# Optimization experiments

Hardware: AMD Instinct MI355X
Metric: run time of the kernel (lower is better)

The kernel has to match this reference:

```python
import jax, jax.numpy as jnp
import numpy as np

NQ, BS, NP_, D = 100, 8, 17, 256
NH, L, P = 8, 4, 4
DH = D // NH
DFF = 1024
SHAPES = [(92, 92), (46, 46), (23, 23), (12, 12)]
LEN_IN = sum(h * w for h, w in SHAPES)


def setup_inputs() -> dict:
    key = jax.random.key(0)
    ks = jax.random.split(key, 20)
    def nrm(k, shape, s=0.02):
        return jax.random.normal(k, shape, jnp.float32) * s
    return {
        "tgt_pose": jax.random.normal(ks[0], (NQ, BS, NP_, D), jnp.float32),
        "tgt_pose_query_pos": jax.random.normal(ks[1], (NQ, BS, NP_, D), jnp.float32),
        "tgt_pose_reference_points": jax.random.uniform(ks[2], (NQ, BS, NP_, L, 2), jnp.float32),
        "memory": jax.random.normal(ks[3], (BS, LEN_IN, D), jnp.float32),
        "w_in_w": nrm(ks[4], (3 * D, D)), "b_in_w": jnp.zeros((3 * D,), jnp.float32),
        "w_out_w": nrm(ks[5], (D, D)), "b_out_w": jnp.zeros((D,), jnp.float32),
        "w_in_a": nrm(ks[6], (3 * D, D)), "b_in_a": jnp.zeros((3 * D,), jnp.float32),
        "w_out_a": nrm(ks[7], (D, D)), "b_out_a": jnp.zeros((D,), jnp.float32),
        "w_off": nrm(ks[8], (NH * L * P * 2, D)), "b_off": nrm(ks[9], (NH * L * P * 2,), 0.1),
        "w_aw": nrm(ks[10], (NH * L * P, D)), "b_aw": jnp.zeros((NH * L * P,), jnp.float32),
        "w_val": nrm(ks[11], (D, D)), "b_val": jnp.zeros((D,), jnp.float32),
        "w_oc": nrm(ks[12], (D, D)), "b_oc": jnp.zeros((D,), jnp.float32),
        "g_w": jnp.ones((D,), jnp.float32), "be_w": jnp.zeros((D,), jnp.float32),
        "g_a": jnp.ones((D,), jnp.float32), "be_a": jnp.zeros((D,), jnp.float32),
        "g1": jnp.ones((D,), jnp.float32), "be1": jnp.zeros((D,), jnp.float32),
        "g2": jnp.ones((D,), jnp.float32), "be2": jnp.zeros((D,), jnp.float32),
        "w1": nrm(ks[13], (DFF, D)), "b1": jnp.zeros((DFF,), jnp.float32),
        "w2": nrm(ks[14], (D, DFF)), "b2": jnp.zeros((D,), jnp.float32),
        "memory_key_padding_mask": jnp.zeros((BS, LEN_IN), jnp.bool_),
        "memory_spatial_shapes": jnp.array(SHAPES, jnp.int32),
        "memory_level_start_index": jnp.array(np.cumsum([0] + [h * w for h, w in SHAPES[:-1]]), jnp.int32),
    }


def _ln(x, g, b, eps=1e-5):
    m = x.mean(-1, keepdims=True)
    v = ((x - m) ** 2).mean(-1, keepdims=True)
    return (x - m) * jax.lax.rsqrt(v + eps) * g + b


def _mha(q, k, v, w_in, b_in, w_out, b_out):
    # q,k,v: [B, S, D] batch-first; torch nn.MultiheadAttention math
    B, S, d = q.shape
    qp = (q @ w_in[:d].T + b_in[:d]).reshape(B, S, NH, DH)
    kp = (k @ w_in[d:2 * d].T + b_in[d:2 * d]).reshape(B, -1, NH, DH)
    vp = (v @ w_in[2 * d:].T + b_in[2 * d:]).reshape(B, -1, NH, DH)
    att = jax.nn.softmax(jnp.einsum('bqhd,bkhd->bhqk', qp, kp) / jnp.sqrt(jnp.float32(DH)), axis=-1)
    o = jnp.einsum('bhqk,bkhd->bqhd', att, vp).reshape(B, S, d)
    return o @ w_out.T + b_out


def _bilinear(v, loc, Hl, Wl):
    # v: [Hl*Wl, NH, DH]; loc: [Lq, NH, P, 2] normalized to [0,1]; grid_sample align_corners=False, zero pad
    x = loc[..., 0] * Wl - 0.5
    y = loc[..., 1] * Hl - 0.5
    x0 = jnp.floor(x); y0 = jnp.floor(y)
    wx = x - x0; wy = y - y0
    x0i = x0.astype(jnp.int32); y0i = y0.astype(jnp.int32)
    hid = jnp.arange(NH)[None, :, None]
    def tap(yi, xi, w):
        ok = (xi >= 0) & (xi < Wl) & (yi >= 0) & (yi < Hl)
        idx = jnp.clip(yi, 0, Hl - 1) * Wl + jnp.clip(xi, 0, Wl - 1)
        return jnp.where(ok[..., None], v[idx, hid], 0.0) * w[..., None]
    return (tap(y0i, x0i, (1 - wy) * (1 - wx)) + tap(y0i, x0i + 1, (1 - wy) * wx)
            + tap(y0i + 1, x0i, wy * (1 - wx)) + tap(y0i + 1, x0i + 1, wy * wx))


def _deform(query, ref, memory, mask, shapes, starts, w_off, b_off, w_aw, b_aw, w_val, b_val, w_oc, b_oc):
    # Multi-scale deformable attention (MSDeformAttn)
    bs, lq, d = query.shape
    value = memory @ w_val.T + b_val
    value = jnp.where(mask[..., None], 0.0, value).reshape(bs, -1, NH, DH)
    off = (query @ w_off.T + b_off).reshape(bs, lq, NH, L, P, 2)
    aw = jax.nn.softmax((query @ w_aw.T + b_aw).reshape(bs, lq, NH, L * P), axis=-1).reshape(bs, lq, NH, L, P)
    shp = np.asarray(shapes)
    st = np.asarray(starts)
    norm = jnp.asarray(shp[:, ::-1].copy(), jnp.float32)  # (W, H) per level
    loc = ref[:, :, None, :, None, :] + off / norm[None, None, None, :, None, :]
    out = jnp.zeros((bs, lq, NH, DH), query.dtype)
    for l in range(L):
        Hl, Wl = int(shp[l, 0]), int(shp[l, 1])
        v_l = value[:, int(st[l]):int(st[l]) + Hl * Wl]
        samp = jax.vmap(lambda vv, lo: _bilinear(vv, lo, Hl, Wl))(v_l, loc[:, :, :, l])
        out = out + jnp.einsum('bqhp,bqhpd->bqhd', aw[:, :, :, l], samp)
    return out.reshape(bs, lq, d) @ w_oc.T + b_oc


def _forward(tgt_pose, qpos, ref, memory, w_in_w, b_in_w, w_out_w, b_out_w, w_in_a, b_in_a, w_out_a, b_out_a, w_off, b_off, w_aw, b_aw, w_val, b_val, w_oc, b_oc, g_w, be_w, g_a, be_a, g1, be1, g2, be2, w1, b1, w2, b2, mask, shapes, starts):
    nq, bs, npt, d = tgt_pose.shape
    # within-group self-attn over keypoints (seq = np, batch = nq*bs)
    qk = (tgt_pose + qpos).reshape(nq * bs, npt, d)
    t2 = _mha(qk, qk, tgt_pose.reshape(nq * bs, npt, d), w_in_w, b_in_w, w_out_w, b_out_w).reshape(nq, bs, npt, d)
    x = _ln(tgt_pose + t2, g_w, be_w)
    # across-group self-attn over queries (seq = nq, batch = bs*np)
    y = x.reshape(nq, bs * npt, d).transpose(1, 0, 2)
    t2 = _mha(y, y, y, w_in_a, b_in_a, w_out_a, b_out_a).transpose(1, 0, 2).reshape(nq, bs, npt, d)
    x = _ln(x + t2, g_a, be_a)
    # multi-scale deformable cross-attn
    q = (x + qpos).transpose(1, 0, 2, 3).reshape(bs, nq * npt, d)
    r = ref.transpose(1, 0, 2, 3, 4).reshape(bs, nq * npt, L, 2)
    t2 = _deform(q, r, memory, mask, shapes, starts, w_off, b_off, w_aw, b_aw, w_val, b_val, w_oc, b_oc)
    t2 = t2.reshape(bs, nq, npt, d).transpose(1, 0, 2, 3)
    x = _ln(x + t2, g1, be1)
    # FFN
    ff = jax.nn.relu(x @ w1.T + b1) @ w2.T + b2
    return _ln(x + ff, g2, be2)


def reference(tgt_pose, tgt_pose_query_pos, tgt_pose_reference_points, memory, w_in_w, b_in_w, w_out_w, b_out_w, w_in_a, b_in_a, w_out_a, b_out_a, w_off, b_off, w_aw, b_aw, w_val, b_val, w_oc, b_oc, g_w, be_w, g_a, be_a, g1, be1, g2, be2, w1, b1, w2, b2, memory_key_padding_mask, memory_spatial_shapes, memory_level_start_index):
    return _forward(tgt_pose, tgt_pose_query_pos, tgt_pose_reference_points, memory, w_in_w, b_in_w, w_out_w, b_out_w, w_in_a, b_in_a, w_out_a, b_out_a, w_off, b_off, w_aw, b_aw, w_val, b_val, w_oc, b_oc, g_w, be_w, g_a, be_a, g1, be1, g2, be2, w1, b1, w2, b2, memory_key_padding_mask, memory_spatial_shapes, memory_level_start_index)
```

## Files before the change

kernel.cpp:

```cpp
#include <hip/hip_runtime.h>
#include <hip/hip_bf16.h>
#include <math.h>

#define NQd 100
#define BSd 8
#define NPTd 17
#define DIMd 256
#define NHd 8
#define DHd 32
#define DFFd 1024
#define NTOK (NQd*BSd*NPTd)
#define LENIN 11253
#define MTOK (BSd*LENIN)

typedef __attribute__((ext_vector_type(8))) short bf16x8;
typedef __attribute__((ext_vector_type(4))) short bf16x4s;
typedef __attribute__((ext_vector_type(4))) float f32x4;

__device__ inline short f2bs(float f) {
    __hip_bfloat16 h = __float2bfloat16(f);
    return *reinterpret_cast<short*>(&h);
}
__device__ inline float bs2f(short s) {
    return __uint_as_float(((unsigned)(unsigned short)s) << 16);
}

template<bool RELU, bool OUT_BF16, bool A_FP32>
__global__ __launch_bounds__(256)
void gemm_mfma(const void* __restrict__ Av, const __hip_bfloat16* __restrict__ W,
               const float* __restrict__ bias, void* __restrict__ Cv,
               int M, int N, int K, int ldc, int col0) {
    __shared__ __hip_bfloat16 LA[2][4][129][8];
    __shared__ __hip_bfloat16 LW[2][4][129][8];
    const int tid = threadIdx.x;
    const int lane = tid & 63, wave = tid >> 6;
    const int wr = wave >> 1, wc = wave & 1;
    const int m0 = blockIdx.y * 128, n0 = blockIdx.x * 128;
    const int l15 = lane & 15, lg = lane >> 4;
    const int srow = tid >> 2, koct = tid & 3;
    bf16x8 aReg[2], wReg[2];

    auto load_tile = [&](int k0) {
#pragma unroll
        for (int it = 0; it < 2; ++it) {
            const int row = srow + it * 64;
            const int gm = m0 + row;
            bf16x8 av = {0, 0, 0, 0, 0, 0, 0, 0};
            if (A_FP32) {
                if (gm < M) {
                    const float* ap = (const float*)Av + (size_t)gm * K + k0 + koct * 8;
                    float4 f0 = *(const float4*)ap;
                    float4 f1 = *(const float4*)(ap + 4);
                    av = (bf16x8){f2bs(f0.x), f2bs(f0.y), f2bs(f0.z), f2bs(f0.w),
                                  f2bs(f1.x), f2bs(f1.y), f2bs(f1.z), f2bs(f1.w)};
                }
            } else {
                if (gm < M)
                    av = *(const bf16x8*)((const __hip_bfloat16*)Av + (size_t)gm * K + k0 + koct * 8);
            }
            aReg[it] = av;
            wReg[it] = *(const bf16x8*)(W + (size_t)(n0 + row) * K + k0 + koct * 8);
        }
    };
    auto write_tile = [&](int buf) {
#pragma unroll
        for (int it = 0; it < 2; ++it) {
            const int row = srow + it * 64;
            *(bf16x8*)&LA[buf][koct][row][0] = aReg[it];
            *(bf16x8*)&LW[buf][koct][row][0] = wReg[it];
        }
    };

    f32x4 acc[4][4];
#pragma unroll
    for (int i = 0; i < 4; ++i)
#pragma unroll
        for (int j = 0; j < 4; ++j) acc[i][j] = (f32x4){0.f, 0.f, 0.f, 0.f};

    const int NT = K >> 5;
    load_tile(0);
    write_tile(0);
    __syncthreads();
    for (int t = 0; t < NT; ++t) {
        const int cur = t & 1;
        if (t + 1 < NT) load_tile((t + 1) * 32);
        bf16x8 af[4], bfr[4];
#pragma unroll
        for (int f = 0; f < 4; ++f) {
            af[f]  = *(const bf16x8*)&LA[cur][lg][wr * 64 + f * 16 + l15][0];
            bfr[f] = *(const bf16x8*)&LW[cur][lg][wc * 64 + f * 16 + l15][0];
        }
#pragma unroll
        for (int fm = 0; fm < 4; ++fm)
#pragma unroll
            for (int fn = 0; fn < 4; ++fn)
                acc[fm][fn] = __builtin_amdgcn_mfma_f32_16x16x32_bf16(af[fm], bfr[fn], acc[fm][fn], 0, 0, 0);
        if (t + 1 < NT) write_tile(cur ^ 1);
        __syncthreads();
    }

#pragma unroll
    for (int fm = 0; fm < 4; ++fm) {
        const int row = m0 + wr * 64 + fm * 16 + lg * 4;
#pragma unroll
        for (int fn = 0; fn < 4; ++fn) {
            const int coln = n0 + wc * 64 + fn * 16 + l15;
            const float bsv = bias[coln];
#pragma unroll
            for (int r = 0; r < 4; ++r) {
                const int gr = row + r;
                if (gr >= M) continue;
                float v = acc[fm][fn][r] + bsv;
                if (RELU) v = fmaxf(v, 0.f);
                if (OUT_BF16)
                    ((__hip_bfloat16*)Cv)[(size_t)gr * ldc + col0 + coln] = __float2bfloat16(v);
                else
                    ((float*)Cv)[(size_t)gr * ldc + col0 + coln] = v;
            }
        }
    }
}

template<bool A_FP32, bool OUT_BF16>
__global__ __launch_bounds__(256)
void gemm64(const void* __restrict__ Av, const __hip_bfloat16* __restrict__ W,
            const float* __restrict__ bias, void* __restrict__ Cv,
            int M, int K, int ldc, int col0) {
    __shared__ __hip_bfloat16 LA[2][4][65][8];
    __shared__ __hip_bfloat16 LW[2][4][65][8];
    const int tid = threadIdx.x;
    const int lane = tid & 63, wave = tid >> 6;
    const int wr = wave >> 1, wc = wave & 1;
    const int m0 = blockIdx.y * 64, n0 = blockIdx.x * 64;
    const int l15 = lane & 15, lg = lane >> 4;
    const int srow = tid >> 2, koct = tid & 3;
    const int gm = m0 + srow;
    const bool okA = gm < M;
    const __hip_bfloat16* pAb = (const __hip_bfloat16*)Av + (size_t)(okA ? gm : 0) * K + koct * 8;
    const float* pAf = (const float*)Av + (size_t)(okA ? gm : 0) * K + koct * 8;
    const __hip_bfloat16* pW = W + (size_t)(n0 + srow) * K + koct * 8;

    bf16x8 aR, wR;
    float4 f0R, f1R;
    auto load_tile = [&](int k0) {
        if (A_FP32) {
            f0R = okA ? *(const float4*)(pAf + k0)     : make_float4(0.f, 0.f, 0.f, 0.f);
            f1R = okA ? *(const float4*)(pAf + k0 + 4) : make_float4(0.f, 0.f, 0.f, 0.f);
        } else {
            aR = okA ? *(const bf16x8*)(pAb + k0) : (bf16x8){0, 0, 0, 0, 0, 0, 0, 0};
        }
        wR = *(const bf16x8*)(pW + k0);
    };
    auto write_tile = [&](int buf) {
        bf16x8 v;
        if (A_FP32)
            v = (bf16x8){f2bs(f0R.x), f2bs(f0R.y), f2bs(f0R.z), f2bs(f0R.w),
                         f2bs(f1R.x), f2bs(f1R.y), f2bs(f1R.z), f2bs(f1R.w)};
        else
            v = aR;
        *(bf16x8*)&LA[buf][koct][srow][0] = v;
        *(bf16x8*)&LW[buf][koct][srow][0] = wR;
    };

    f32x4 acc[2][2];
#pragma unroll
    for (int i = 0; i < 2; ++i)
#pragma unroll
        for (int j = 0; j < 2; ++j) acc[i][j] = (f32x4){0.f, 0.f, 0.f, 0.f};

    const int NT = K >> 5;
    load_tile(0);
    write_tile(0);
    __syncthreads();
    for (int t = 0; t < NT; ++t) {
        const int cur = t & 1;
        if (t + 1 < NT) load_tile((t + 1) * 32);
        bf16x8 af[2], bfr[2];
#pragma unroll
        for (int f = 0; f < 2; ++f) {
            af[f]  = *(const bf16x8*)&LA[cur][lg][wr * 32 + f * 16 + l15][0];
            bfr[f] = *(const bf16x8*)&LW[cur][lg][wc * 32 + f * 16 + l15][0];
        }
#pragma unroll
        for (int fm = 0; fm < 2; ++fm)
#pragma unroll
            for (int fn = 0; fn < 2; ++fn)
                acc[fm][fn] = __builtin_amdgcn_mfma_f32_16x16x32_bf16(af[fm], bfr[fn], acc[fm][fn], 0, 0, 0);
        if (t + 1 < NT) write_tile(cur ^ 1);
        __syncthreads();
    }

#pragma unroll
    for (int fm = 0; fm < 2; ++fm) {
        const int row = m0 + wr * 32 + fm * 16 + lg * 4;
#pragma unroll
        for (int fn = 0; fn < 2; ++fn) {
            const int coln = n0 + wc * 32 + fn * 16 + l15;
            const float bsv = bias[coln];
#pragma unroll
            for (int r = 0; r < 4; ++r) {
                const int gr = row + r;
                if (gr >= M) continue;
                float v = acc[fm][fn][r] + bsv;
                if (OUT_BF16)
                    ((__hip_bfloat16*)Cv)[(size_t)gr * ldc + col0 + coln] = __float2bfloat16(v);
                else
                    ((float*)Cv)[(size_t)gr * ldc + col0 + coln] = v;
            }
        }
    }
}

__global__ __launch_bounds__(256)
void gemm64x(const float* __restrict__ Av, const __hip_bfloat16* __restrict__ W,
             const float* __restrict__ bias, __hip_bfloat16* __restrict__ Cv,
             int M, int K, int ldc) {
    const int nwg = gridDim.x;
    const int orig = blockIdx.x;
    const int xcd = orig & 7, loc = orig >> 3;
    const int q = nwg >> 3, r = nwg & 7;
    const int swz = (xcd < r ? xcd * (q + 1) : r * (q + 1) + (xcd - r) * q) + loc;
    const int m0 = (swz >> 2) * 64, n0 = (swz & 3) * 64;

    __shared__ __hip_bfloat16 LA[2][4][65][8];
    __shared__ __hip_bfloat16 LW[2][4][65][8];
    const int tid = threadIdx.x;
    const int lane = tid & 63, wave = tid >> 6;
    const int wr = wave >> 1, wc = wave & 1;
    const int l15 = lane & 15, lg = lane >> 4;
    const int srow = tid >> 2, koct = tid & 3;
    const int gm = m0 + srow;
    const bool okA = gm < M;
    const float* pAf = Av + (size_t)(okA ? gm : 0) * K + koct * 8;
    const __hip_bfloat16* pW = W + (size_t)(n0 + srow) * K + koct * 8;

    bf16x8 wR;
    float4 f0R, f1R;
    auto load_tile = [&](int k0) {
        f0R = okA ? *(const float4*)(pAf + k0)     : make_float4(0.f, 0.f, 0.f, 0.f);
        f1R = okA ? *(const float4*)(pAf + k0 + 4) : make_float4(0.f, 0.f, 0.f, 0.f);
        wR = *(const bf16x8*)(pW + k0);
    };
    auto write_tile = [&](int buf) {
        *(bf16x8*)&LA[buf][koct][srow][0] =
            (bf16x8){f2bs(f0R.x), f2bs(f0R.y), f2bs(f0R.z), f2bs(f0R.w),
                     f2bs(f1R.x), f2bs(f1R.y), f2bs(f1R.z), f2bs(f1R.w)};
        *(bf16x8*)&LW[buf][koct][srow][0] = wR;
    };

    f32x4 acc[2][2];
#pragma unroll
    for (int i = 0; i < 2; ++i)
#pragma unroll
        for (int j = 0; j < 2; ++j) acc[i][j] = (f32x4){0.f, 0.f, 0.f, 0.f};

    const int NT = K >> 5;
    load_tile(0);
    write_tile(0);
    __syncthreads();
    for (int t = 0; t < NT; ++t) {
        const int cur = t & 1;
        if (t + 1 < NT) load_tile((t + 1) * 32);
        bf16x8 af[2], bfr[2];
#pragma unroll
        for (int f = 0; f < 2; ++f) {
            af[f]  = *(const bf16x8*)&LA[cur][lg][wr * 32 + f * 16 + l15][0];
            bfr[f] = *(const bf16x8*)&LW[cur][lg][wc * 32 + f * 16 + l15][0];
        }
#pragma unroll
        for (int fm = 0; fm < 2; ++fm)
#pragma unroll
            for (int fn = 0; fn < 2; ++fn)
                acc[fm][fn] = __builtin_amdgcn_mfma_f32_16x16x32_bf16(af[fm], bfr[fn], acc[fm][fn], 0, 0, 0);
        if (t + 1 < NT) write_tile(cur ^ 1);
        __syncthreads();
    }

#pragma unroll
    for (int fm = 0; fm < 2; ++fm) {
        const int row = m0 + wr * 32 + fm * 16 + lg * 4;
#pragma unroll
        for (int fn = 0; fn < 2; ++fn) {
            const int coln = n0 + wc * 32 + fn * 16 + l15;
            const float bsv = bias[coln];
#pragma unroll
            for (int r = 0; r < 4; ++r) {
                const int gr = row + r;
                if (gr >= M) continue;
                Cv[(size_t)gr * ldc + coln] = __float2bfloat16(acc[fm][fn][r] + bsv);
            }
        }
    }
}

__global__ void cvt_weights(const float* w0, const float* w1, const float* w2,
                            const float* w3, const float* w4, const float* w5,
                            const float* w6, const float* w7, const float* w8,
                            const float* w9, __hip_bfloat16* dst) {
    int idx = blockIdx.x * 256 + threadIdx.x;
    float v;
    if      (idx <  196608) v = w0[idx];
    else if (idx <  262144) v = w1[idx -  196608];
    else if (idx <  458752) v = w2[idx -  262144];
    else if (idx <  524288) v = w3[idx -  458752];
    else if (idx <  589824) v = w4[idx -  524288];
    else if (idx <  622592) v = w5[idx -  589824];
    else if (idx <  688128) v = w6[idx -  622592];
    else if (idx <  753664) v = w7[idx -  688128];
    else if (idx < 1015808) v = w8[idx -  753664];
    else                    v = w9[idx - 1015808];
    dst[idx] = __float2bfloat16(v);
}

__global__ void gather_rows_b(const float* __restrict__ src, const float* __restrict__ add,
                              __hip_bfloat16* __restrict__ dst, int mode) {
    int t = blockIdx.x, c = threadIdx.x;
    int r;
    if (mode == 0) r = t;
    else if (mode == 1) { int m = t / 100, q = t % 100; r = q * 136 + m; }
    else { int b = t / 1700, jj = t % 1700; int q = jj / 17, p = jj % 17; r = q * 136 + b * 17 + p; }
    float v = src[(size_t)r * 256 + c];
    if (add) v += add[(size_t)r * 256 + c];
    dst[(size_t)t * 256 + c] = __float2bfloat16(v);
}

__global__ void attn17(const __hip_bfloat16* __restrict__ qkv, __hip_bfloat16* __restrict__ out) {
    const int g = blockIdx.x, h = blockIdx.y;
    __shared__ float q[17][32], k[17][32], v[17][32], s[17][18];
    const int tid = threadIdx.x;
    for (int idx = tid; idx < 17 * 32; idx += 256) {
        int i = idx >> 5, d = idx & 31;
        size_t row = (size_t)(g * 17 + i) * 768 + h * 32 + d;
        q[i][d] = bs2f(*(const short*)&qkv[row]);
        k[i][d] = bs2f(*(const short*)&qkv[row + 256]);
        v[i][d] = bs2f(*(const short*)&qkv[row + 512]);
    }
    __syncthreads();
    for (int idx = tid; idx < 17 * 17; idx += 256) {
        int i = idx / 17, j = idx % 17;
        float acc = 0.f;
#pragma unroll
        for (int d = 0; d < 32; ++d) acc += q[i][d] * k[j][d];
        s[i][j] = acc * 0.17677669529663688f;
    }
    __syncthreads();
    if (tid < 17) {
        float m = -1e30f;
        for (int j = 0; j < 17; ++j) m = fmaxf(m, s[tid][j]);
        float sum = 0.f;
        for (int j = 0; j < 17; ++j) { float e = __expf(s[tid][j] - m); s[tid][j] = e; sum += e; }
        float inv = 1.f / sum;
        for (int j = 0; j < 17; ++j) s[tid][j] *= inv;
    }
    __syncthreads();
    for (int idx = tid; idx < 17 * 32; idx += 256) {
        int i = idx >> 5, d = idx & 31;
        float acc = 0.f;
        for (int j = 0; j < 17; ++j) acc += s[i][j] * v[j][d];
        out[(size_t)(g * 17 + i) * 256 + h * 32 + d] = __float2bfloat16(acc);
    }
}

__global__ __launch_bounds__(128)
void attn100(const __hip_bfloat16* __restrict__ qkv, __hip_bfloat16* __restrict__ out) {
    const int g = blockIdx.x, h = blockIdx.y;
    __shared__ __hip_bfloat16 Vt[32][136];
    __shared__ __hip_bfloat16 Pl[2][16][136];
    const int tid = threadIdx.x;
    const int wave = tid >> 6, lane = tid & 63;
    const int l15 = lane & 15, lg = lane >> 4;

    for (int idx = tid; idx < 3200; idx += 128) {
        int j = idx >> 5, d = idx & 31;
        Vt[d][j] = qkv[(size_t)(g * 100 + j) * 768 + 512 + h * 32 + d];
    }
    for (int idx = tid; idx < 32 * 28; idx += 128) {
        int d = idx & 31, jz = 100 + (idx >> 5);
        Vt[d][jz] = __float2bfloat16(0.f);
    }
    __syncthreads();

    const int rt0 = wave ? 4 : 0, rt1 = wave ? 7 : 4;
    for (int rt = rt0; rt < rt1; ++rt) {
        const int rowbase = rt * 16;
        int qr = rowbase + l15; if (qr > 99) qr = 99;
        bf16x8 aq = *(const bf16x8*)(qkv + (size_t)(g * 100 + qr) * 768 + h * 32 + lg * 8);
        f32x4 s[7];
#pragma unroll
        for (int jt = 0; jt < 7; ++jt) {
            int jr = jt * 16 + l15; if (jr > 99) jr = 99;
            bf16x8 bk = *(const bf16x8*)(qkv + (size_t)(g * 100 + jr) * 768 + 256 + h * 32 + lg * 8);
            s[jt] = __builtin_amdgcn_mfma_f32_16x16x32_bf16(aq, bk, (f32x4){0.f, 0.f, 0.f, 0.f}, 0, 0, 0);
        }
        float mr[4] = {-1e30f, -1e30f, -1e30f, -1e30f};
#pragma unroll
        for (int jt = 0; jt < 7; ++jt) {
            const bool valid = (jt * 16 + l15) < 100;
#pragma unroll
            for (int r = 0; r < 4; ++r) {
                float v = valid ? s[jt][r] * 0.17677669529663688f : -1e30f;
                s[jt][r] = v;
                mr[r] = fmaxf(mr[r], v);
            }
        }
#pragma unroll
        for (int r = 0; r < 4; ++r) {
            mr[r] = fmaxf(mr[r], __shfl_xor(mr[r], 1));
            mr[r] = fmaxf(mr[r], __shfl_xor(mr[r], 2));
            mr[r] = fmaxf(mr[r], __shfl_xor(mr[r], 4));
            mr[r] = fmaxf(mr[r], __shfl_xor(mr[r], 8));
        }
        float lr[4] = {0.f, 0.f, 0.f, 0.f};
#pragma unroll
        for (int jt = 0; jt < 7; ++jt)
#pragma unroll
            for (int r = 0; r < 4; ++r) {
                float e = __expf(s[jt][r] - mr[r]);
                s[jt][r] = e;
                lr[r] += e;
            }
#pragma unroll
        for (int r = 0; r < 4; ++r) {
            lr[r] += __shfl_xor(lr[r], 1);
            lr[r] += __shfl_xor(lr[r], 2);
            lr[r] += __shfl_xor(lr[r], 4);
            lr[r] += __shfl_xor(lr[r], 8);
        }
#pragma unroll
        for (int jt = 0; jt < 7; ++jt)
#pragma unroll
            for (int r = 0; r < 4; ++r)
                Pl[wave][lg * 4 + r][jt * 16 + l15] = __float2bfloat16(s[jt][r]);
#pragma unroll
        for (int r = 0; r < 4; ++r)
            Pl[wave][lg * 4 + r][112 + l15] = __float2bfloat16(0.f);

        f32x4 o0 = (f32x4){0.f, 0.f, 0.f, 0.f};
        f32x4 o1 = (f32x4){0.f, 0.f, 0.f, 0.f};
#pragma unroll
        for (int c = 0; c < 4; ++c) {
            bf16x8 pa = *(const bf16x8*)&Pl[wave][l15][c * 32 + lg * 8];
            bf16x8 v0 = *(const bf16x8*)&Vt[l15][c * 32 + lg * 8];
            bf16x8 v1 = *(const bf16x8*)&Vt[16 + l15][c * 32 + lg * 8];
            o0 = __builtin_amdgcn_mfma_f32_16x16x32_bf16(pa, v0, o0, 0, 0, 0);
            o1 = __builtin_amdgcn_mfma_f32_16x16x32_bf16(pa, v1, o1, 0, 0, 0);
        }
#pragma unroll
        for (int r = 0; r < 4; ++r) {
            int row = rowbase + lg * 4 + r;
            if (row < 100) {
                float inv = 1.f / lr[r];
                __hip_bfloat16* op = out + (size_t)(g * 100 + row) * 256 + h * 32;
                op[l15]      = __float2bfloat16(o0[r] * inv);
                op[16 + l15] = __float2bfloat16(o1[r] * inv);
            }
        }
    }
}

#define TPB 4
__global__ __launch_bounds__(256)
void deform_sample(const __hip_bfloat16* __restrict__ value, const float* __restrict__ off,
                   const float* __restrict__ aw, const float* __restrict__ ref,
                   __hip_bfloat16* __restrict__ out) {
    const int t0 = blockIdx.x * TPB;
    const int tid = threadIdx.x;
    __shared__ float raw[TPB][128];
    __shared__ float wgt[TPB][128];
    __shared__ int   cidx[TPB][128][4];
    __shared__ float cw[TPB][128][4];

    for (int idx = tid; idx < TPB * 128; idx += 256) {
        int tk = idx >> 7, i = idx & 127;
        raw[tk][i] = aw[(size_t)(t0 + tk) * 128 + i];
    }
    __syncthreads();
    if (tid < TPB * 8) {
        int tk = tid >> 3, h = tid & 7;
        float m = -1e30f;
        for (int i = 0; i < 16; ++i) m = fmaxf(m, raw[tk][h * 16 + i]);
        float sum = 0.f;
        float e[16];
        for (int i = 0; i < 16; ++i) { e[i] = __expf(raw[tk][h * 16 + i] - m); sum += e[i]; }
        float inv = 1.f / sum;
        for (int i = 0; i < 16; ++i) wgt[tk][h * 16 + i] = e[i] * inv;
    }
    __syncthreads();

    const int Hs[4] = {92, 46, 23, 12};
    const int Sts[4] = {0, 8464, 10580, 11109};
    for (int s = tid; s < TPB * 128; s += 256) {
        int tk = s >> 7, sid = s & 127;
        int t = t0 + tk;
        int b = t / 1700, jj = t % 1700;
        int q = jj / 17, p = jj % 17;
        int l = (sid >> 2) & 3;
        int HW = Hs[l];
        float HWf = (float)HW;
        const float* refp = ref + (size_t)((q * 8 + b) * 17 + p) * 8;
        float rx = refp[l * 2], ry = refp[l * 2 + 1];
        float ox = off[(size_t)t * 256 + sid * 2];
        float oy = off[(size_t)t * 256 + sid * 2 + 1];
        float x = (rx + ox / HWf) * HWf - 0.5f;
        float y = (ry + oy / HWf) * HWf - 0.5f;
        float x0f = floorf(x), y0f = floorf(y);
        float wx = x - x0f, wy = y - y0f;
        int xi = (int)x0f, yi = (int)y0f;
        float wg = wgt[tk][sid];
#pragma unroll
        for (int c = 0; c < 4; ++c) {
            int cy = c >> 1, cx = c & 1;
            int yy = yi + cy, xx = xi + cx;
            bool ok = (xx >= 0) && (xx < HW) && (yy >= 0) && (yy < HW);
            int yc = min(max(yy, 0), HW - 1);
            int xc = min(max(xx, 0), HW - 1);
            cidx[tk][sid][c] = Sts[l] + yc * HW + xc;
            float w = (cy ? wy : 1.f - wy) * (cx ? wx : 1.f - wx);
            cw[tk][sid][c] = ok ? wg * w : 0.f;
        }
    }
    __syncthreads();

    const int tk = tid >> 6, lane = tid & 63;
    const int h = lane >> 3, d4 = (lane & 7) * 4;
    const int t = t0 + tk;
    const int b = t / 1700;
    const __hip_bfloat16* vb = value + (size_t)b * LENIN * 256 + h * 32 + d4;
    float4 acc = make_float4(0.f, 0.f, 0.f, 0.f);
    for (int s16 = 0; s16 < 16; ++s16) {
        int sid = h * 16 + s16;
#pragma unroll
        for (int c = 0; c < 4; ++c) {
            int idx = cidx[tk][sid][c];
            float w = cw[tk][sid][c];
            bf16x4s v = *(const bf16x4s*)(vb + (size_t)idx * 256);
            acc.x += w * bs2f(v.x); acc.y += w * bs2f(v.y);
            acc.z += w * bs2f(v.z); acc.w += w * bs2f(v.w);
        }
    }
    __hip_bfloat16* op = out + (size_t)t * 256 + h * 32 + d4;
    op[0] = __float2bfloat16(acc.x);
    op[1] = __float2bfloat16(acc.y);
    op[2] = __float2bfloat16(acc.z);
    op[3] = __float2bfloat16(acc.w);
}

__global__ __launch_bounds__(256)
void res_ln(const float* __restrict__ res, const float* __restrict__ proj,
            const float* __restrict__ g, const float* __restrict__ be,
            float* __restrict__ out, __hip_bfloat16* __restrict__ outb, int mode) {
    const int wave = threadIdx.x >> 6, lane = threadIdx.x & 63;
    const int r = blockIdx.x * 4 + wave;
    int t;
    if (mode == 0) t = r;
    else if (mode == 1) { int q = r / 136, m = r % 136; t = m * 100 + q; }
    else { int q = r / 136, rem = r % 136; int b = rem / 17, p = rem % 17; t = b * 1700 + q * 17 + p; }
    const int c4 = lane * 4;
    float4 a = *(const float4*)&res[(size_t)r * 256 + c4];
    float4 p = *(const float4*)&proj[(size_t)t * 256 + c4];
    float v[4] = {a.x + p.x, a.y + p.y, a.z + p.z, a.w + p.w};
    float s = v[0] + v[1] + v[2] + v[3];
#pragma unroll
    for (int off = 32; off > 0; off >>= 1) s += __shfl_xor(s, off);
    float mean = s * (1.f / 256.f);
    float d[4], ss = 0.f;
#pragma unroll
    for (int i = 0; i < 4; ++i) { d[i] = v[i] - mean; ss += d[i] * d[i]; }
#pragma unroll
    for (int off = 32; off > 0; off >>= 1) ss += __shfl_xor(ss, off);
    float rs = rsqrtf(ss * (1.f / 256.f) + 1e-5f);
    float4 gv = *(const float4*)&g[c4];
    float4 bv = *(const float4*)&be[c4];
    float o0 = d[0] * rs * gv.x + bv.x;
    float o1 = d[1] * rs * gv.y + bv.y;
    float o2 = d[2] * rs * gv.z + bv.z;
    float o3 = d[3] * rs * gv.w + bv.w;
    *(float4*)&out[(size_t)r * 256 + c4] = make_float4(o0, o1, o2, o3);
    if (outb) {
        bf16x4s ob = {f2bs(o0), f2bs(o1), f2bs(o2), f2bs(o3)};
        *(bf16x4s*)&outb[(size_t)r * 256 + c4] = ob;
    }
}

extern "C" void kernel_launch(void* const* d_in, const int* in_sizes, int n_in,
                              void* d_out, int out_size, void* d_ws, size_t ws_size,
                              hipStream_t stream) {
    const float* tgt    = (const float*)d_in[0];
    const float* qpos   = (const float*)d_in[1];
    const float* ref    = (const float*)d_in[2];
    const float* memory = (const float*)d_in[3];
    const float* w_in_w = (const float*)d_in[4];
    const float* b_in_w = (const float*)d_in[5];
    const float* w_out_w= (const float*)d_in[6];
    const float* b_out_w= (const float*)d_in[7];
    const float* w_in_a = (const float*)d_in[8];
    const float* b_in_a = (const float*)d_in[9];
    const float* w_out_a= (const float*)d_in[10];
    const float* b_out_a= (const float*)d_in[11];
    const float* w_off  = (const float*)d_in[12];
    const float* b_off  = (const float*)d_in[13];
    const float* w_aw   = (const float*)d_in[14];
    const float* b_aw   = (const float*)d_in[15];
    const float* w_val  = (const float*)d_in[16];
    const float* b_val  = (const float*)d_in[17];
    const float* w_oc   = (const float*)d_in[18];
    const float* b_oc   = (const float*)d_in[19];
    const float* g_w    = (const float*)d_in[20];
    const float* be_w   = (const float*)d_in[21];
    const float* g_a    = (const float*)d_in[22];
    const float* be_a   = (const float*)d_in[23];
    const float* g1     = (const float*)d_in[24];
    const float* be1    = (const float*)d_in[25];
    const float* g2     = (const float*)d_in[26];
    const float* be2    = (const float*)d_in[27];
    const float* w1     = (const float*)d_in[28];
    const float* b1     = (const float*)d_in[29];
    const float* w2     = (const float*)d_in[30];
    const float* b2     = (const float*)d_in[31];

    float* X  = (float*)d_out;
    float* ws = (float*)d_ws;
    float* R1 = ws;
    float* R2 = R1 + (size_t)MTOK * 256;
    float* R3 = R2 + (size_t)NTOK * 256;
    float* R6 = R3 + (size_t)NTOK * 128;
    float* QBF= R6 + (size_t)NTOK * 128;
    float* WBF= QBF+ (size_t)NTOK * 128;

    __hip_bfloat16* R1b = (__hip_bfloat16*)R1;
    __hip_bfloat16* R3b = (__hip_bfloat16*)R3;
    __hip_bfloat16* Qb  = (__hip_bfloat16*)QBF;
    __hip_bfloat16* Wb  = (__hip_bfloat16*)WBF;
    __hip_bfloat16* Hb  = (__hip_bfloat16*)R1;
    __hip_bfloat16* Vb  = (__hip_bfloat16*)R1;

    __hip_bfloat16* w_in_w_b  = Wb;
    __hip_bfloat16* w_out_w_b = Wb +  196608;
    __hip_bfloat16* w_in_a_b  = Wb +  262144;
    __hip_bfloat16* w_out_a_b = Wb +  458752;
    __hip_bfloat16* w_off_b   = Wb +  524288;
    __hip_bfloat16* w_aw_b    = Wb +  589824;
    __hip_bfloat16* w_val_b   = Wb +  622592;
    __hip_bfloat16* w_oc_b    = Wb +  688128;
    __hip_bfloat16* w1_b      = Wb +  753664;
    __hip_bfloat16* w2_b      = Wb + 1015808;

    cvt_weights<<<4992, 256, 0, stream>>>(w_in_w, w_out_w, w_in_a, w_out_a, w_off,
                                          w_aw, w_val, w_oc, w1, w2, Wb);

    const int MY64 = (NTOK + 63) / 64;

    gather_rows_b<<<NTOK, 256, 0, stream>>>(tgt, qpos, Qb, 0);
    gemm_mfma<false, true, false><<<dim3(4, (NTOK + 127) / 128), 256, 0, stream>>>(
        Qb, w_in_w_b, b_in_w, R1b, NTOK, 512, 256, 768, 0);
    gemm64<true, true><<<dim3(4, MY64), 256, 0, stream>>>(
        tgt, w_in_w_b + 512 * 256, b_in_w + 512, R1b, NTOK, 256, 768, 512);
    attn17<<<dim3(800, 8), 256, 0, stream>>>(R1b, R3b);
    gemm64<false, false><<<dim3(4, MY64), 256, 0, stream>>>(
        R3b, w_out_w_b, b_out_w, R2, NTOK, 256, 256, 0);
    res_ln<<<NTOK / 4, 256, 0, stream>>>(tgt, R2, g_w, be_w, X, nullptr, 0);

    gather_rows_b<<<NTOK, 256, 0, stream>>>(X, nullptr, Qb, 1);
    gemm_mfma<false, true, false><<<dim3(6, (NTOK + 127) / 128), 256, 0, stream>>>(
        Qb, w_in_a_b, b_in_a, R1b, NTOK, 768, 256, 768, 0);
    attn100<<<dim3(136, 8), 128, 0, stream>>>(R1b, R3b);
    gemm64<false, false><<<dim3(4, MY64), 256, 0, stream>>>(
        R3b, w_out_a_b, b_out_a, R2, NTOK, 256, 256, 0);
    res_ln<<<NTOK / 4, 256, 0, stream>>>(X, R2, g_a, be_a, X, nullptr, 1);

    gemm64x<<<4 * ((MTOK + 63) / 64), 256, 0, stream>>>(
        memory, w_val_b, b_val, Vb, MTOK, 256, 256);
    gather_rows_b<<<NTOK, 256, 0, stream>>>(X, qpos, Qb, 2);
    gemm64<false, false><<<dim3(4, MY64), 256, 0, stream>>>(
        Qb, w_off_b, b_off, R2, NTOK, 256, 256, 0);
    gemm64<false, false><<<dim3(2, MY64), 256, 0, stream>>>(
        Qb, w_aw_b, b_aw, R6, NTOK, 256, 128, 0);
    deform_sample<<<NTOK / TPB, 256, 0, stream>>>(Vb, R2, R6, ref, R3b);
    gemm64<false, false><<<dim3(4, MY64), 256, 0, stream>>>(
        R3b, w_oc_b, b_oc, R2, NTOK, 256, 256, 0);
    res_ln<<<NTOK / 4, 256, 0, stream>>>(X, R2, g1, be1, X, Qb, 2);

    gemm_mfma<true, true, false><<<dim3(8, (NTOK + 127) / 128), 256, 0, stream>>>(
        Qb, w1_b, b1, Hb, NTOK, 1024, 256, 1024, 0);
    gemm64<false, false><<<dim3(4, MY64), 256, 0, stream>>>(
        (const __hip_bfloat16*)Hb, w2_b, b2, R2, NTOK, 1024, 256, 0);
    res_ln<<<NTOK / 4, 256, 0, stream>>>(X, R2, g2, be2, X, nullptr, 0);
}
```

Before: 326.6 us.

## Fuse row gathers into GEMM A-loads and drop the 128-tile GEMM

Removes the separate gather_rows_b kernels. Their permutation and the query-pos add now happen inside the GEMM A-tile load (AMAP modes), which saves a bf16 round trip through global memory per projection. The offset and attention-weight projections are merged into one kernel that writes to two outputs. All 128x128 gemm_mfma launches become 64x64 gemm64 launches with more blocks, which trades data reuse per block for more parallelism. The fused paths read fp32 activations on every N-block, so redundant global reads and per-row index math increase.

```diff
diff --git a/kernel.cpp b/kernel.cpp
--- a/kernel.cpp
+++ b/kernel.cpp
@@ -25,107 +25,11 @@
     return __uint_as_float(((unsigned)(unsigned short)s) << 16);
 }
 
-template<bool RELU, bool OUT_BF16, bool A_FP32>
+template<int AMAP, bool OUT_BF16, bool RELU>
 __global__ __launch_bounds__(256)
-void gemm_mfma(const void* __restrict__ Av, const __hip_bfloat16* __restrict__ W,
-               const float* __restrict__ bias, void* __restrict__ Cv,
-               int M, int N, int K, int ldc, int col0) {
-    __shared__ __hip_bfloat16 LA[2][4][129][8];
-    __shared__ __hip_bfloat16 LW[2][4][129][8];
-    const int tid = threadIdx.x;
-    const int lane = tid & 63, wave = tid >> 6;
-    const int wr = wave >> 1, wc = wave & 1;
-    const int m0 = blockIdx.y * 128, n0 = blockIdx.x * 128;
-    const int l15 = lane & 15, lg = lane >> 4;
-    const int srow = tid >> 2, koct = tid & 3;
-    bf16x8 aReg[2], wReg[2];
-
-    auto load_tile = [&](int k0) {
-#pragma unroll
-        for (int it = 0; it < 2; ++it) {
-            const int row = srow + it * 64;
-            const int gm = m0 + row;
-            bf16x8 av = {0, 0, 0, 0, 0, 0, 0, 0};
-            if (A_FP32) {
-                if (gm < M) {
-                    const float* ap = (const float*)Av + (size_t)gm * K + k0 + koct * 8;
-                    float4 f0 = *(const float4*)ap;
-                    float4 f1 = *(const float4*)(ap + 4);
-                    av = (bf16x8){f2bs(f0.x), f2bs(f0.y), f2bs(f0.z), f2bs(f0.w),
-                                  f2bs(f1.x), f2bs(f1.y), f2bs(f1.z), f2bs(f1.w)};
-                }
-            } else {
-                if (gm < M)
-                    av = *(const bf16x8*)((const __hip_bfloat16*)Av + (size_t)gm * K + k0 + koct * 8);
-            }
-            aReg[it] = av;
-            wReg[it] = *(const bf16x8*)(W + (size_t)(n0 + row) * K + k0 + koct * 8);
-        }
-    };
-    auto write_tile = [&](int buf) {
-#pragma unroll
-        for (int it = 0; it < 2; ++it) {
-            const int row = srow + it * 64;
-            *(bf16x8*)&LA[buf][koct][row][0] = aReg[it];
-            *(bf16x8*)&LW[buf][koct][row][0] = wReg[it];
-        }
-    };
-
-    f32x4 acc[4][4];
-#pragma unroll
-    for (int i = 0; i < 4; ++i)
-#pragma unroll
-        for (int j = 0; j < 4; ++j) acc[i][j] = (f32x4){0.f, 0.f, 0.f, 0.f};
-
-    const int NT = K >> 5;
-    load_tile(0);
-    write_tile(0);
-    __syncthreads();
-    for (int t = 0; t < NT; ++t) {
-        const int cur = t & 1;
-        if (t + 1 < NT) load_tile((t + 1) * 32);
-        bf16x8 af[4], bfr[4];
-#pragma unroll
-        for (int f = 0; f < 4; ++f) {
-            af[f]  = *(const bf16x8*)&LA[cur][lg][wr * 64 + f * 16 + l15][0];
-            bfr[f] = *(const bf16x8*)&LW[cur][lg][wc * 64 + f * 16 + l15][0];
-        }
-#pragma unroll
-        for (int fm = 0; fm < 4; ++fm)
-#pragma unroll
-            for (int fn = 0; fn < 4; ++fn)
-                acc[fm][fn] = __builtin_amdgcn_mfma_f32_16x16x32_bf16(af[fm], bfr[fn], acc[fm][fn], 0, 0, 0);
-        if (t + 1 < NT) write_tile(cur ^ 1);
-        __syncthreads();
-    }
-
-#pragma unroll
-    for (int fm = 0; fm < 4; ++fm) {
-        const int row = m0 + wr * 64 + fm * 16 + lg * 4;
-#pragma unroll
-        for (int fn = 0; fn < 4; ++fn) {
-            const int coln = n0 + wc * 64 + fn * 16 + l15;
-            const float bsv = bias[coln];
-#pragma unroll
-            for (int r = 0; r < 4; ++r) {
-                const int gr = row + r;
-                if (gr >= M) continue;
-                float v = acc[fm][fn][r] + bsv;
-                if (RELU) v = fmaxf(v, 0.f);
-                if (OUT_BF16)
-                    ((__hip_bfloat16*)Cv)[(size_t)gr * ldc + col0 + coln] = __float2bfloat16(v);
-                else
-                    ((float*)Cv)[(size_t)gr * ldc + col0 + coln] = v;
-            }
-        }
-    }
-}
-
-template<bool A_FP32, bool OUT_BF16>
-__global__ __launch_bounds__(256)
-void gemm64(const void* __restrict__ Av, const __hip_bfloat16* __restrict__ W,
-            const float* __restrict__ bias, void* __restrict__ Cv,
-            int M, int K, int ldc, int col0) {
+void gemm64(const void* __restrict__ Av, const float* __restrict__ Aadd,
+            const __hip_bfloat16* __restrict__ W, const float* __restrict__ bias,
+            void* __restrict__ Cv, int M, int K, int ldc, int col0) {
     __shared__ __hip_bfloat16 LA[2][4][65][8];
     __shared__ __hip_bfloat16 LW[2][4][65][8];
     const int tid = threadIdx.x;
@@ -136,28 +40,41 @@
     const int srow = tid >> 2, koct = tid & 3;
     const int gm = m0 + srow;
     const bool okA = gm < M;
-    const __hip_bfloat16* pAb = (const __hip_bfloat16*)Av + (size_t)(okA ? gm : 0) * K + koct * 8;
-    const float* pAf = (const float*)Av + (size_t)(okA ? gm : 0) * K + koct * 8;
+    int src = okA ? gm : 0;
+    if (AMAP == 3) src = (src % 100) * 136 + src / 100;
+    const __hip_bfloat16* pAb = (const __hip_bfloat16*)Av + (size_t)src * K + koct * 8;
+    const float* pAf = (const float*)Av + (size_t)src * K + koct * 8;
+    const float* pDf = (AMAP == 2) ? (Aadd + (size_t)src * K + koct * 8) : nullptr;
     const __hip_bfloat16* pW = W + (size_t)(n0 + srow) * K + koct * 8;
 
     bf16x8 aR, wR;
-    float4 f0R, f1R;
+    float4 f0R, f1R, d0R, d1R;
     auto load_tile = [&](int k0) {
-        if (A_FP32) {
+        if (AMAP == 0) {
+            aR = okA ? *(const bf16x8*)(pAb + k0) : (bf16x8){0, 0, 0, 0, 0, 0, 0, 0};
+        } else {
             f0R = okA ? *(const float4*)(pAf + k0)     : make_float4(0.f, 0.f, 0.f, 0.f);
             f1R = okA ? *(const float4*)(pAf + k0 + 4) : make_float4(0.f, 0.f, 0.f, 0.f);
-        } else {
-            aR = okA ? *(const bf16x8*)(pAb + k0) : (bf16x8){0, 0, 0, 0, 0, 0, 0, 0};
+            if (AMAP == 2) {
+                d0R = okA ? *(const float4*)(pDf + k0)     : make_float4(0.f, 0.f, 0.f, 0.f);
+                d1R = okA ? *(const float4*)(pDf + k0 + 4) : make_float4(0.f, 0.f, 0.f, 0.f);
+            }
         }
         wR = *(const bf16x8*)(pW + k0);
     };
     auto write_tile = [&](int buf) {
         bf16x8 v;
-        if (A_FP32)
-            v = (bf16x8){f2bs(f0R.x), f2bs(f0R.y), f2bs(f0R.z), f2bs(f0R.w),
-                         f2bs(f1R.x), f2bs(f1R.y), f2bs(f1R.z), f2bs(f1R.w)};
-        else
+        if (AMAP == 0) {
             v = aR;
+        } else {
+            float4 f0 = f0R, f1 = f1R;
+            if (AMAP == 2) {
+                f0.x += d0R.x; f0.y += d0R.y; f0.z += d0R.z; f0.w += d0R.w;
+                f1.x += d1R.x; f1.y += d1R.y; f1.z += d1R.z; f1.w += d1R.w;
+            }
+            v = (bf16x8){f2bs(f0.x), f2bs(f0.y), f2bs(f0.z), f2bs(f0.w),
+                         f2bs(f1.x), f2bs(f1.y), f2bs(f1.z), f2bs(f1.w)};
+        }
         *(bf16x8*)&LA[buf][koct][srow][0] = v;
         *(bf16x8*)&LW[buf][koct][srow][0] = wR;
     };
@@ -202,10 +119,102 @@
                 const int gr = row + r;
                 if (gr >= M) continue;
                 float v = acc[fm][fn][r] + bsv;
+                if (RELU) v = fmaxf(v, 0.f);
                 if (OUT_BF16)
                     ((__hip_bfloat16*)Cv)[(size_t)gr * ldc + col0 + coln] = __float2bfloat16(v);
                 else
                     ((float*)Cv)[(size_t)gr * ldc + col0 + coln] = v;
+            }
+        }
+    }
+}
+
+__global__ __launch_bounds__(256)
+void gemm64qa(const float* __restrict__ X, const float* __restrict__ qpos,
+              const __hip_bfloat16* __restrict__ W,
+              const float* __restrict__ boff, const float* __restrict__ baw,
+              float* __restrict__ Coff, float* __restrict__ Caw, int M, int K) {
+    __shared__ __hip_bfloat16 LA[2][4][65][8];
+    __shared__ __hip_bfloat16 LW[2][4][65][8];
+    const int tid = threadIdx.x;
+    const int lane = tid & 63, wave = tid >> 6;
+    const int wr = wave >> 1, wc = wave & 1;
+    const int m0 = blockIdx.y * 64, n0 = blockIdx.x * 64;
+    const int l15 = lane & 15, lg = lane >> 4;
+    const int srow = tid >> 2, koct = tid & 3;
+    const int gm = m0 + srow;
+    const bool okA = gm < M;
+    int t_ = okA ? gm : 0;
+    {
+        int b = t_ / 1700, jj = t_ % 1700;
+        int qq = jj / 17, p = jj % 17;
+        t_ = qq * 136 + b * 17 + p;
+    }
+    const float* pAf = X + (size_t)t_ * K + koct * 8;
+    const float* pDf = qpos + (size_t)t_ * K + koct * 8;
+    const __hip_bfloat16* pW = W + (size_t)(n0 + srow) * K + koct * 8;
+
+    bf16x8 wR;
+    float4 f0R, f1R, d0R, d1R;
+    auto load_tile = [&](int k0) {
+        f0R = okA ? *(const float4*)(pAf + k0)     : make_float4(0.f, 0.f, 0.f, 0.f);
+        f1R = okA ? *(const float4*)(pAf + k0 + 4) : make_float4(0.f, 0.f, 0.f, 0.f);
+        d0R = okA ? *(const float4*)(pDf + k0)     : make_float4(0.f, 0.f, 0.f, 0.f);
+        d1R = okA ? *(const float4*)(pDf + k0 + 4) : make_float4(0.f, 0.f, 0.f, 0.f);
+        wR = *(const bf16x8*)(pW + k0);
+    };
+    auto write_tile = [&](int buf) {
+        *(bf16x8*)&LA[buf][koct][srow][0] =
+            (bf16x8){f2bs(f0R.x + d0R.x), f2bs(f0R.y + d0R.y),
+                     f2bs(f0R.z + d0R.z), f2bs(f0R.w + d0R.w),
+                     f2bs(f1R.x + d1R.x), f2bs(f1R.y + d1R.y),
+                     f2bs(f1R.z + d1R.z), f2bs(f1R.w + d1R.w)};
+        *(bf16x8*)&LW[buf][koct][srow][0] = wR;
+    };
+
+    f32x4 acc[2][2];
+#pragma unroll
+    for (int i = 0; i < 2; ++i)
+#pragma unroll
+        for (int j = 0; j < 2; ++j) acc[i][j] = (f32x4){0.f, 0.f, 0.f, 0.f};
+
+    const int NT = K >> 5;
+    load_tile(0);
+    write_tile(0);
+    __syncthreads();
+    for (int t = 0; t < NT; ++t) {
+        const int cur = t & 1;
+        if (t + 1 < NT) load_tile((t + 1) * 32);
+        bf16x8 af[2], bfr[2];
+#pragma unroll
+        for (int f = 0; f < 2; ++f) {
+            af[f]  = *(const bf16x8*)&LA[cur][lg][wr * 32 + f * 16 + l15][0];
+            bfr[f] = *(const bf16x8*)&LW[cur][lg][wc * 32 + f * 16 + l15][0];
+        }
+#pragma unroll
+        for (int fm = 0; fm < 2; ++fm)
+#pragma unroll
+            for (int fn = 0; fn < 2; ++fn)
+                acc[fm][fn] = __builtin_amdgcn_mfma_f32_16x16x32_bf16(af[fm], bfr[fn], acc[fm][fn], 0, 0, 0);
+        if (t + 1 < NT) write_tile(cur ^ 1);
+        __syncthreads();
+    }
+
+#pragma unroll
+    for (int fm = 0; fm < 2; ++fm) {
+        const int row = m0 + wr * 32 + fm * 16 + lg * 4;
+#pragma unroll
+        for (int fn = 0; fn < 2; ++fn) {
+            const int coln = n0 + wc * 32 + fn * 16 + l15;
+#pragma unroll
+            for (int r = 0; r < 4; ++r) {
+                const int gr = row + r;
+                if (gr >= M) continue;
+                if (coln < 256) {
+                    Coff[(size_t)gr * 256 + coln] = acc[fm][fn][r] + boff[coln];
+                } else {
+                    Caw[(size_t)gr * 128 + (coln - 256)] = acc[fm][fn][r] + baw[coln - 256];
+                }
             }
         }
     }
@@ -310,18 +319,6 @@
     else if (idx < 1015808) v = w8[idx -  753664];
     else                    v = w9[idx - 1015808];
     dst[idx] = __float2bfloat16(v);
-}
-
-__global__ void gather_rows_b(const float* __restrict__ src, const float* __restrict__ add,
-                              __hip_bfloat16* __restrict__ dst, int mode) {
-    int t = blockIdx.x, c = threadIdx.x;
-    int r;
-    if (mode == 0) r = t;
-    else if (mode == 1) { int m = t / 100, q = t % 100; r = q * 136 + m; }
-    else { int b = t / 1700, jj = t % 1700; int q = jj / 17, p = jj % 17; r = q * 136 + b * 17 + p; }
-    float v = src[(size_t)r * 256 + c];
-    if (add) v += add[(size_t)r * 256 + c];
-    dst[(size_t)t * 256 + c] = __float2bfloat16(v);
 }
 
 __global__ void attn17(const __hip_bfloat16* __restrict__ qkv, __hip_bfloat16* __restrict__ out) {
@@ -650,39 +647,34 @@
 
     const int MY64 = (NTOK + 63) / 64;
 
-    gather_rows_b<<<NTOK, 256, 0, stream>>>(tgt, qpos, Qb, 0);
-    gemm_mfma<false, true, false><<<dim3(4, (NTOK + 127) / 128), 256, 0, stream>>>(
-        Qb, w_in_w_b, b_in_w, R1b, NTOK, 512, 256, 768, 0);
-    gemm64<true, true><<<dim3(4, MY64), 256, 0, stream>>>(
-        tgt, w_in_w_b + 512 * 256, b_in_w + 512, R1b, NTOK, 256, 768, 512);
+    gemm64<2, true, false><<<dim3(8, MY64), 256, 0, stream>>>(
+        tgt, qpos, w_in_w_b, b_in_w, R1b, NTOK, 256, 768, 0);
+    gemm64<1, true, false><<<dim3(4, MY64), 256, 0, stream>>>(
+        tgt, nullptr, w_in_w_b + 512 * 256, b_in_w + 512, R1b, NTOK, 256, 768, 512);
     attn17<<<dim3(800, 8), 256, 0, stream>>>(R1b, R3b);
-    gemm64<false, false><<<dim3(4, MY64), 256, 0, stream>>>(
-        R3b, w_out_w_b, b_out_w, R2, NTOK, 256, 256, 0);
+    gemm64<0, false, false><<<dim3(4, MY64), 256, 0, stream>>>(
+        R3b, nullptr, w_out_w_b, b_out_w, R2, NTOK, 256, 256, 0);
     res_ln<<<NTOK / 4, 256, 0, stream>>>(tgt, R2, g_w, be_w, X, nullptr, 0);
 
-    gather_rows_b<<<NTOK, 256, 0, stream>>>(X, nullptr, Qb, 1);
-    gemm_mfma<false, true, false><<<dim3(6, (NTOK + 127) / 128), 256, 0, stream>>>(
-        Qb, w_in_a_b, b_in_a, R1b, NTOK, 768, 256, 768, 0);
+    gemm64<3, true, false><<<dim3(12, MY64), 256, 0, stream>>>(
+        X, nullptr, w_in_a_b, b_in_a, R1b, NTOK, 256, 768, 0);
     attn100<<<dim3(136, 8), 128, 0, stream>>>(R1b, R3b);
-    gemm64<false, false><<<dim3(4, MY64), 256, 0, stream>>>(
-        R3b, w_out_a_b, b_out_a, R2, NTOK, 256, 256, 0);
+    gemm64<0, false, false><<<dim3(4, MY64), 256, 0, stream>>>(
+        R3b, nullptr, w_out_a_b, b_out_a, R2, NTOK, 256, 256, 0);
     res_ln<<<NTOK / 4, 256, 0, stream>>>(X, R2, g_a, be_a, X, nullptr, 1);
 
     gemm64x<<<4 * ((MTOK + 63) / 64), 256, 0, stream>>>(
         memory, w_val_b, b_val, Vb, MTOK, 256, 256);
-    gather_rows_b<<<NTOK, 256, 0, stream>>>(X, qpos, Qb, 2);
-    gemm64<false, false><<<dim3(4, MY64), 256, 0, stream>>>(
-        Qb, w_off_b, b_off, R2, NTOK, 256, 256, 0);
-    gemm64<false, false><<<dim3(2, MY64), 256, 0, stream>>>(
-        Qb, w_aw_b, b_aw, R6, NTOK, 256, 128, 0);
+    gemm64qa<<<dim3(6, MY64), 256, 0, stream>>>(
+        X, qpos, w_off_b, b_off, b_aw, R2, R6, NTOK, 256);
     deform_sample<<<NTOK / TPB, 256, 0, stream>>>(Vb, R2, R6, ref, R3b);
-    gemm64<false, false><<<dim3(4, MY64), 256, 0, stream>>>(
-        R3b, w_oc_b, b_oc, R2, NTOK, 256, 256, 0);
+    gemm64<0, false, false><<<dim3(4, MY64), 256, 0, stream>>>(
+        R3b, nullptr, w_oc_b, b_oc, R2, NTOK, 256, 256, 0);
     res_ln<<<NTOK / 4, 256, 0, stream>>>(X, R2, g1, be1, X, Qb, 2);
 
-    gemm_mfma<true, true, false><<<dim3(8, (NTOK + 127) / 128), 256, 0, stream>>>(
-        Qb, w1_b, b1, Hb, NTOK, 1024, 256, 1024, 0);
-    gemm64<false, false><<<dim3(4, MY64), 256, 0, stream>>>(
-        (const __hip_bfloat16*)Hb, w2_b, b2, R2, NTOK, 1024, 256, 0);
+    gemm64<0, true, true><<<dim3(16, MY64), 256, 0, stream>>>(
+        Qb, nullptr, w1_b, b1, Hb, NTOK, 256, 1024, 0);
+    gemm64<0, false, false><<<dim3(4, MY64), 256, 0, stream>>>(
+        Hb, nullptr, w2_b, b2, R2, NTOK, 1024, 256, 0);
     res_ln<<<NTOK / 4, 256, 0, stream>>>(X, R2, g2, be2, X, nullptr, 0);
 }
```

Result: slower. 350.0 us (+7.1%).
